# Optimization experiments

Hardware: AMD Instinct MI355X
Metric: run time of the kernel (lower is better)

## Reference

```python
import jax, jax.numpy as jnp
import numpy as np

D_IN = 4097   # 4096 obj feat + 1 depth
D_H1 = 512
D_H2 = 256
N_HEADS = 4
D_HEAD = D_H2 // N_HEADS
D_FF = 512


def setup_inputs() -> dict:
    key = jax.random.key(0)
    ks = jax.random.split(key, 20)
    B, T, N = 2, 100, 30
    s = lambda *sh: 1.0 / np.sqrt(sh[0])
    inp = {
        "object_features": jax.random.normal(ks[0], (B, T, N, 4096), jnp.float32),
        "object_depths": jax.random.uniform(ks[1], (B, T, N, 1), jnp.float32),
        # spatial encoder (2-layer fully-connected message passing)
        "W1a": jax.random.normal(ks[2], (D_IN, D_H1), jnp.float32) * s(D_IN),
        "W2a": jax.random.normal(ks[3], (D_IN, D_H1), jnp.float32) * s(D_IN),
        "b1a": jnp.zeros((D_H1,), jnp.float32),
        "W1b": jax.random.normal(ks[4], (D_H1, D_H2), jnp.float32) * s(D_H1),
        "W2b": jax.random.normal(ks[5], (D_H1, D_H2), jnp.float32) * s(D_H1),
        "b1b": jnp.zeros((D_H2,), jnp.float32),
        # temporal transformer encoder layer (post-LN)
        "Wq": jax.random.normal(ks[6], (D_H2, D_H2), jnp.float32) * s(D_H2),
        "Wk": jax.random.normal(ks[7], (D_H2, D_H2), jnp.float32) * s(D_H2),
        "Wv": jax.random.normal(ks[8], (D_H2, D_H2), jnp.float32) * s(D_H2),
        "Wo": jax.random.normal(ks[9], (D_H2, D_H2), jnp.float32) * s(D_H2),
        "ln1_g": jnp.ones((D_H2,), jnp.float32),
        "ln1_b": jnp.zeros((D_H2,), jnp.float32),
        "Wf1": jax.random.normal(ks[10], (D_H2, D_FF), jnp.float32) * s(D_H2),
        "bf1": jnp.zeros((D_FF,), jnp.float32),
        "Wf2": jax.random.normal(ks[11], (D_FF, D_H2), jnp.float32) * s(D_FF),
        "bf2": jnp.zeros((D_H2,), jnp.float32),
        "ln2_g": jnp.ones((D_H2,), jnp.float32),
        "ln2_b": jnp.zeros((D_H2,), jnp.float32),
        # classifier
        "Wc": jax.random.normal(ks[12], (D_H2, 1), jnp.float32) * s(D_H2),
        "bc": jnp.zeros((1,), jnp.float32),
    }
    return inp


def _layer_norm(x, g, b, eps=1e-5):
    mu = jnp.mean(x, axis=-1, keepdims=True)
    var = jnp.var(x, axis=-1, keepdims=True)
    return (x - mu) * jax.lax.rsqrt(var + eps) * g + b


def _forward(object_features, object_depths, W1a, W2a, b1a, W1b, W2b, b1b,
             Wq, Wk, Wv, Wo, ln1_g, ln1_b, Wf1, bf1, Wf2, bf2, ln2_g, ln2_b,
             Wc, bc):
    B, T, N, _ = object_features.shape
    x = jnp.concatenate([object_features, object_depths], axis=-1)  # (B,T,N,4097)
    # fully-connected graph (torch.combinations, both directions):
    # aggregated message for node i = mean over all j != i.
    def mp(h, Ws, Wn, b):
        neigh = (jnp.sum(h, axis=2, keepdims=True) - h) / (N - 1)
        return jax.nn.relu(h @ Ws + neigh @ Wn + b)
    h = mp(x, W1a, W2a, b1a)      # (B,T,N,512)
    h = mp(h, W1b, W2b, b1b)      # (B,T,N,256)
    g = jnp.mean(h, axis=2)       # global mean pool -> (B,T,256)
    # temporal transformer encoder (self-attention over T, post-LN)
    q = (g @ Wq).reshape(B, T, N_HEADS, D_HEAD)
    k = (g @ Wk).reshape(B, T, N_HEADS, D_HEAD)
    v = (g @ Wv).reshape(B, T, N_HEADS, D_HEAD)
    scores = jnp.einsum("bthd,bshd->bhts", q, k) / np.sqrt(D_HEAD)
    attn = jax.nn.softmax(scores, axis=-1)
    ctx = jnp.einsum("bhts,bshd->bthd", attn, v).reshape(B, T, D_H2) @ Wo
    y = _layer_norm(g + ctx, ln1_g, ln1_b)
    ff = jax.nn.relu(y @ Wf1 + bf1) @ Wf2 + bf2
    z = _layer_norm(y + ff, ln2_g, ln2_b)  # (B,T,256)
    # dropout is identity in eval mode -> probs2 == probs, uncertainty == 0
    logits = (z @ Wc + bc).squeeze(-1)     # (B,T)
    probs = jax.nn.sigmoid(logits)
    uncertainty = jnp.zeros_like(probs)
    return probs, uncertainty


def reference(object_features, object_depths, W1a, W2a, b1a, W1b, W2b, b1b,
              Wq, Wk, Wv, Wo, ln1_g, ln1_b, Wf1, bf1, Wf2, bf2, ln2_g, ln2_b,
              Wc, bc):
    return _forward(object_features, object_depths, W1a, W2a, b1a, W1b, W2b,
                    b1b, Wq, Wk, Wv, Wo, ln1_g, ln1_b, Wf1, bf1, Wf2, bf2,
                    ln2_g, ln2_b, Wc, bc)
```

## Files before the change

### kernel.cpp

```cpp
#include <hip/hip_runtime.h>
#include <hip/hip_bf16.h>
#include <stdint.h>

typedef unsigned short u16;
typedef __attribute__((ext_vector_type(8))) short short8;
typedef __attribute__((ext_vector_type(4))) float floatx4;
typedef __attribute__((ext_vector_type(4))) unsigned short ushort4_t;

#define BT 200
#define NOBJ 30
#define KP2 4224
#define DIN 4097
#define DH1 512
#define DH2 256
#define DFF 512
#define MPAD 6016
#define CHZ 176
#define NBIGW (132*16)
#define NSMALL 512
#define NCONV (BT*3)
#define NZERO 128

__device__ __forceinline__ u16 f2bf(float f) {
    union { float f; uint32_t u; } c; c.f = f;
    uint32_t u = c.u;
    u += 0x7FFF + ((u >> 16) & 1);
    return (u16)(u >> 16);
}

__device__ __forceinline__ void load16_lds(const u16* g, u16* l) {
    __builtin_amdgcn_global_load_lds(
        (const __attribute__((address_space(1))) void*)g,
        (__attribute__((address_space(3))) void*)l, 16, 0, 0);
}

__device__ __forceinline__ size_t tile_off(int ytile, int row, int c8) {
    int z = c8 / CHZ, rem = c8 - z * CHZ;
    int i = rem >> 3, kw = rem & 7;
    int ks = kw ^ (row & 7);
    return ((((size_t)(ytile * 3 + z) * 22 + i) * 128 + row) * 64) + ks * 8;
}

__global__ void prep_all(const float* __restrict__ W1a, const float* __restrict__ W2a,
                         const float* __restrict__ W1b, const float* __restrict__ W2b,
                         const float* __restrict__ feat, const float* __restrict__ depth,
                         u16* __restrict__ Wc1T, u16* __restrict__ W2aTs,
                         u16* __restrict__ Wc2T, u16* __restrict__ W2bTs,
                         u16* __restrict__ XbT, u16* __restrict__ SbT,
                         float* __restrict__ zeroBase, size_t zeroQuads) {
    __shared__ float t1[32][33];
    __shared__ float t2[32][33];
    int bid = blockIdx.x, tid = threadIdx.x;
    if (bid < NCONV) {
        int bt = bid / 3;
        int c8 = (bid % 3) * 256 + tid;
        if (c8 >= 528) return;
        int k8 = c8 * 8;
        int zc = c8 / CHZ, rem = c8 - zc * CHZ;
        int ic = rem >> 3, kwc = rem & 7;
        float s[8] = {};
        if (k8 < 4096) {
            const float* fb = feat + (size_t)bt * NOBJ * 4096 + k8;
            #pragma unroll 1
            for (int n0 = 0; n0 < NOBJ; n0 += 6) {
                float4 va[6], vb[6];
                #pragma unroll
                for (int u = 0; u < 6; u++) {
                    const float* p = fb + (size_t)(n0 + u) * 4096;
                    va[u] = *(const float4*)p;
                    vb[u] = *(const float4*)(p + 4);
                }
                #pragma unroll
                for (int u = 0; u < 6; u++) {
                    int r = bt * NOBJ + n0 + u;
                    float v[8] = {va[u].x, va[u].y, va[u].z, va[u].w,
                                  vb[u].x, vb[u].y, vb[u].z, vb[u].w};
                    short8 o;
                    #pragma unroll
                    for (int e = 0; e < 8; e++) { s[e] += v[e]; o[e] = (short)f2bf(v[e]); }
                    size_t off = ((((size_t)((r >> 7) * 3 + zc) * 22 + ic) * 128
                                   + (r & 127)) * 64) + (size_t)(kwc ^ (r & 7)) * 8;
                    *(short8*)(XbT + off) = o;
                }
            }
        } else {
            for (int n = 0; n < NOBJ; n++) {
                int r = bt * NOBJ + n;
                short8 o = {};
                if (k8 == 4096) {
                    float d = depth[r];
                    s[0] += d;
                    o[0] = (short)f2bf(d);
                }
                size_t off = ((((size_t)((r >> 7) * 3 + zc) * 22 + ic) * 128
                               + (r & 127)) * 64) + (size_t)(kwc ^ (r & 7)) * 8;
                *(short8*)(XbT + off) = o;
            }
        }
        short8 so;
        #pragma unroll
        for (int e = 0; e < 8; e++) so[e] = (short)f2bf(s[e]);
        {
            int r = bt;
            size_t off = ((((size_t)((r >> 7) * 3 + zc) * 22 + ic) * 128
                           + (r & 127)) * 64) + (size_t)(kwc ^ (r & 7)) * 8;
            *(short8*)(SbT + off) = so;
        }
    } else if (bid < NCONV + NZERO) {
        int zid = bid - NCONV;
        float4* p = (float4*)zeroBase;
        float4 zz = {0.f, 0.f, 0.f, 0.f};
        for (size_t idx = (size_t)zid * 256 + tid; idx < zeroQuads; idx += (size_t)NZERO * 256)
            p[idx] = zz;
    } else if (bid < NCONV + NZERO + NSMALL) {
        int idx = (bid - NCONV - NZERO) * 256 + tid;
        int j = idx >> 9, k = idx & 511;
        float a = W1b[k * DH2 + j];
        float b = W2b[k * DH2 + j] * (1.f / 29.f);
        Wc2T[j * DH1 + k]  = f2bf(a - b);
        W2bTs[j * DH1 + k] = f2bf(b);
    } else {
        int b2 = bid - NCONV - NZERO - NSMALL;
        int kb = (b2 % 132) * 32, jb = (b2 / 132) * 32;
        int tx = tid & 31, ty = tid >> 5;
        #pragma unroll
        for (int r = 0; r < 32; r += 8) {
            int k = kb + ty + r, j = jb + tx;
            float a = 0.f, b = 0.f;
            if (k < DIN) { a = W1a[k * DH1 + j]; b = W2a[k * DH1 + j]; }
            float bs = b * (1.f / 29.f);
            t1[ty + r][tx] = a - bs;
            t2[ty + r][tx] = bs;
        }
        __syncthreads();
        #pragma unroll
        for (int r = 0; r < 32; r += 8) {
            int j = jb + ty + r, k = kb + tx;
            int x = j >> 7, row = j & 127;
            size_t off = tile_off(x, row, k >> 3) + (k & 7);
            Wc1T[off]  = f2bf(t1[tx][ty + r]);
            W2aTs[off] = f2bf(t2[tx][ty + r]);
        }
    }
}

__global__ __launch_bounds__(256) void gemmA(
    const u16* __restrict__ XbT, const u16* __restrict__ WaT,
    const u16* __restrict__ SbT, const u16* __restrict__ WsT,
    float* __restrict__ hacc, float* __restrict__ uOut) {
    __shared__ __align__(16) u16 Al[8192];
    __shared__ __align__(16) u16 Bl[8192];
    int bid = blockIdx.x;
    const u16 *Abase, *Bbase;
    float* outF;
    int m0, n0, M;
    if (bid < 564) {
        int xcd = bid & 7, slot = bid >> 3;
        int lid = (xcd < 4 ? xcd * 71 : 284 + (xcd - 4) * 70) + slot;
        int x = lid & 3, y = (lid >> 2) % 47, z = lid / 188;
        Abase = XbT + (size_t)((y * 3 + z) * 22) * 8192;
        Bbase = WaT + (size_t)((x * 3 + z) * 22) * 8192;
        outF = hacc; M = 6000; m0 = y * 128; n0 = x * 128;
    } else {
        int rem = bid - 564;
        int x = rem & 3, y = (rem >> 2) & 1, z = rem >> 3;
        Abase = SbT + (size_t)((y * 3 + z) * 22) * 8192;
        Bbase = WsT + (size_t)((x * 3 + z) * 22) * 8192;
        outF = uOut; M = BT; m0 = y * 128; n0 = x * 128;
    }
    int tid = threadIdx.x, lane = tid & 63, w = tid >> 6;
    floatx4 acc[4][4] = {};
    int lrow = lane & 15, q = lane >> 4;
    int wm = (w & 1) * 64, wn = (w >> 1) * 64;
    int swz = lrow & 7;

    for (int i = 0; i < 22; i++) {
        const u16* as = Abase + (size_t)i * 8192;
        const u16* bs = Bbase + (size_t)i * 8192;
        #pragma unroll
        for (int it = 0; it < 4; it++) {
            load16_lds(as + (it * 256 + tid) * 8, Al + it * 2048 + w * 512);
            load16_lds(bs + (it * 256 + tid) * 8, Bl + it * 2048 + w * 512);
        }
        __syncthreads();
        #pragma unroll
        for (int h = 0; h < 2; h++) {
            int ci = h * 4 + q;
            int so = (ci ^ swz) * 8;
            short8 af[4], bfv[4];
            #pragma unroll
            for (int ii = 0; ii < 4; ii++)
                af[ii] = *(short8*)(Al + (wm + ii * 16 + lrow) * 64 + so);
            #pragma unroll
            for (int j = 0; j < 4; j++)
                bfv[j] = *(short8*)(Bl + (wn + j * 16 + lrow) * 64 + so);
            #pragma unroll
            for (int ii = 0; ii < 4; ii++)
                #pragma unroll
                for (int j = 0; j < 4; j++)
                    acc[ii][j] = __builtin_amdgcn_mfma_f32_16x16x32_bf16(af[ii], bfv[j], acc[ii][j], 0, 0, 0);
        }
        __syncthreads();
    }

    #pragma unroll
    for (int ii = 0; ii < 4; ii++)
        #pragma unroll
        for (int j = 0; j < 4; j++)
            #pragma unroll
            for (int r = 0; r < 4; r++) {
                int row = m0 + wm + ii * 16 + q * 4 + r;
                int col = n0 + wn + j * 16 + lrow;
                if (row < M)
                    atomicAdd(&outF[(size_t)row * DH1 + col], acc[ii][j][r]);
            }
}

__global__ __launch_bounds__(256) void gemmB(
    const u16* __restrict__ hb, const u16* __restrict__ Wc2T,
    const u16* __restrict__ Shb, const u16* __restrict__ W2bTs,
    float* __restrict__ hacc2, float* __restrict__ u2Out) {
    __shared__ __align__(16) u16 Al[64 * 64];
    __shared__ __align__(16) u16 Bl[128 * 64];
    int bid = blockIdx.x;
    const u16 *A, *B;
    float* outF;
    int m0, n0, kbeg, M;
    if (bid < 376) {
        int xcd = bid & 7, slot = bid >> 3;
        int lid = xcd * 47 + slot;
        int x = lid & 1, y = (lid >> 1) % 94, z = lid / 188;
        A = hb; B = Wc2T; outF = hacc2; M = 6000;
        m0 = y * 64; n0 = x * 128; kbeg = z * 256;
    } else {
        int rem = bid - 376;
        int x = rem & 1, y = (rem >> 1) & 3, z = rem >> 3;
        A = Shb; B = W2bTs; outF = u2Out; M = BT;
        m0 = y * 64; n0 = x * 128; kbeg = z * 256;
    }
    int kend = kbeg + 256;
    const int N = DH2, K = DH1;
    int tid = threadIdx.x;
    int lane = tid & 63, w = tid >> 6;
    int srow = tid >> 3, kslot = tid & 7;
    floatx4 acc[2][4] = {};
    int lrow = lane & 15, q = lane >> 4;
    int wm = (w & 1) * 32, wn = (w >> 1) * 64;
    int swz = lrow & 7;

    for (int kb = kbeg; kb < kend; kb += 64) {
        #pragma unroll
        for (int it = 0; it < 2; it++) {
            int row = it * 32 + srow;
            int kph = kslot ^ (row & 7);
            load16_lds(A + (size_t)(m0 + row) * K + kb + kph * 8,
                       Al + it * 2048 + w * 512);
        }
        #pragma unroll
        for (int it = 0; it < 4; it++) {
            int row = it * 32 + srow;
            int kph = kslot ^ (row & 7);
            load16_lds(B + (size_t)(n0 + row) * K + kb + kph * 8,
                       Bl + it * 2048 + w * 512);
        }
        __syncthreads();
        #pragma unroll
        for (int h = 0; h < 2; h++) {
            int ci = h * 4 + q;
            int so = (ci ^ swz) * 8;
            short8 af[2], bfv[4];
            #pragma unroll
            for (int i = 0; i < 2; i++)
                af[i] = *(short8*)(Al + (wm + i * 16 + lrow) * 64 + so);
            #pragma unroll
            for (int j = 0; j < 4; j++)
                bfv[j] = *(short8*)(Bl + (wn + j * 16 + lrow) * 64 + so);
            #pragma unroll
            for (int i = 0; i < 2; i++)
                #pragma unroll
                for (int j = 0; j < 4; j++)
                    acc[i][j] = __builtin_amdgcn_mfma_f32_16x16x32_bf16(af[i], bfv[j], acc[i][j], 0, 0, 0);
        }
        __syncthreads();
    }

    #pragma unroll
    for (int i = 0; i < 2; i++)
        #pragma unroll
        for (int j = 0; j < 4; j++)
            #pragma unroll
            for (int r = 0; r < 4; r++) {
                int row = m0 + wm + i * 16 + q * 4 + r;
                int col = n0 + wn + j * 16 + lrow;
                if (row < M)
                    atomicAdd(&outF[(size_t)row * N + col], acc[i][j][r]);
            }
}

__global__ void reduce1(const float* __restrict__ hacc, const float* __restrict__ u,
                        const float* __restrict__ b1a,
                        u16* __restrict__ hb, u16* __restrict__ Shb) {
    __shared__ float sl[128];
    int bt = blockIdx.x, c0 = blockIdx.y * 128;
    int lc = threadIdx.x & 127, rp = threadIdx.x >> 7;
    int col = c0 + lc;
    float ub = u[bt * DH1 + col] + b1a[col];
    float s = 0.f;
    for (int n = rp; n < NOBJ; n += 2) {
        float v = hacc[(size_t)(bt * NOBJ + n) * DH1 + col] + ub;
        v = v > 0.f ? v : 0.f;
        hb[(size_t)(bt * NOBJ + n) * DH1 + col] = f2bf(v);
        s += v;
    }
    if (rp == 0) sl[lc] = s;
    __syncthreads();
    if (rp == 1) Shb[bt * DH1 + col] = f2bf(sl[lc] + s);
}

__global__ void reduce2_qkv(const float* __restrict__ hacc2, const float* __restrict__ u2,
                            const float* __restrict__ b1b,
                            const float* __restrict__ Wq, const float* __restrict__ Wk,
                            const float* __restrict__ Wv,
                            float* __restrict__ g, float* __restrict__ q,
                            float* __restrict__ k, float* __restrict__ v) {
    __shared__ float gl[DH2];
    int bt = blockIdx.x, j = threadIdx.x;
    float ub = u2[bt * DH2 + j] + b1b[j];
    float a = 0.f;
    for (int n = 0; n < NOBJ; n++) {
        float vv = hacc2[(size_t)(bt * NOBJ + n) * DH2 + j] + ub;
        a += vv > 0.f ? vv : 0.f;
    }
    a *= (1.f / 30.f);
    gl[j] = a;
    g[bt * DH2 + j] = a;
    __syncthreads();
    float aq = 0.f, ak = 0.f, av = 0.f;
    for (int kk = 0; kk < DH2; kk++) {
        float x = gl[kk];
        aq += x * Wq[kk * DH2 + j];
        ak += x * Wk[kk * DH2 + j];
        av += x * Wv[kk * DH2 + j];
    }
    q[bt * DH2 + j] = aq;
    k[bt * DH2 + j] = ak;
    v[bt * DH2 + j] = av;
}

__device__ __forceinline__ float block_sum256(float v, volatile float* red) {
    #pragma unroll
    for (int o = 32; o > 0; o >>= 1) v += __shfl_down(v, o);
    int w = threadIdx.x >> 6;
    __syncthreads();
    if ((threadIdx.x & 63) == 0) red[w] = v;
    __syncthreads();
    return red[0] + red[1] + red[2] + red[3];
}

__global__ void attn_head(const float* __restrict__ qg, const float* __restrict__ kg,
                          const float* __restrict__ vg, const float* __restrict__ g,
                          const float* __restrict__ Wo,
                          const float* __restrict__ ln1g, const float* __restrict__ ln1b,
                          const float* __restrict__ Wf1, const float* __restrict__ bf1,
                          const float* __restrict__ Wf2, const float* __restrict__ bf2,
                          const float* __restrict__ ln2g, const float* __restrict__ ln2b,
                          const float* __restrict__ Wc, const float* __restrict__ bc,
                          float* __restrict__ out) {
    __shared__ float ql[DH2];
    __shared__ float scl[4][128];
    __shared__ float ctxl[DH2];
    __shared__ float yl[DH2];
    __shared__ float ffl[DFF];
    __shared__ float red[4];
    int row = blockIdx.x, tid = threadIdx.x;
    int base = (row >= 100) ? 100 : 0;
    ql[tid] = qg[row * DH2 + tid];
    __syncthreads();

    for (int p = tid; p < 512; p += 256) {
        int h = p >> 7, s = p & 127;
        if (s < 100) {
            const float* kr = kg + (size_t)(base + s) * DH2 + h * 64;
            float a = 0.f;
            #pragma unroll 8
            for (int d = 0; d < 64; d++) a += ql[h * 64 + d] * kr[d];
            scl[h][s] = a * 0.125f;
        }
    }
    __syncthreads();

    {
        int w = tid >> 6, lane = tid & 63;
        int s2 = 64 + lane;
        float a  = scl[w][lane];
        float b2 = (s2 < 100) ? scl[w][s2] : -1e30f;
        float m = fmaxf(a, b2);
        #pragma unroll
        for (int o = 32; o > 0; o >>= 1) m = fmaxf(m, __shfl_down(m, o));
        m = __shfl(m, 0);
        float e1 = __expf(a - m);
        float e2 = (s2 < 100) ? __expf(b2 - m) : 0.f;
        float sm = e1 + e2;
        #pragma unroll
        for (int o = 32; o > 0; o >>= 1) sm += __shfl_down(sm, o);
        sm = __shfl(sm, 0);
        float r = 1.f / sm;
        scl[w][lane] = e1 * r;
        if (s2 < 100) scl[w][s2] = e2 * r;
    }
    __syncthreads();

    {
        int h = tid >> 6;
        float o = 0.f;
        for (int s = 0; s < 100; s++)
            o += scl[h][s] * vg[(size_t)(base + s) * DH2 + tid];
        ctxl[tid] = o;
    }
    __syncthreads();

    float o = 0.f;
    for (int kk = 0; kk < DH2; kk++) o += ctxl[kk] * Wo[kk * DH2 + tid];
    float t = g[row * DH2 + tid] + o;
    float mu  = block_sum256(t, red) * (1.f / DH2);
    float ex2 = block_sum256(t * t, red) * (1.f / DH2);
    float y = (t - mu) * rsqrtf(ex2 - mu * mu + 1e-5f) * ln1g[tid] + ln1b[tid];
    yl[tid] = y;
    __syncthreads();
    for (int jj = tid; jj < DFF; jj += 256) {
        float a = bf1[jj];
        for (int kk = 0; kk < DH2; kk++) a += yl[kk] * Wf1[kk * DFF + jj];
        ffl[jj] = a > 0.f ? a : 0.f;
    }
    __syncthreads();
    float o2 = bf2[tid];
    for (int kk = 0; kk < DFF; kk++) o2 += ffl[kk] * Wf2[kk * DH2 + tid];
    float z0 = y + o2;
    float mu2  = block_sum256(z0, red) * (1.f / DH2);
    float ex22 = block_sum256(z0 * z0, red) * (1.f / DH2);
    float z = (z0 - mu2) * rsqrtf(ex22 - mu2 * mu2 + 1e-5f) * ln2g[tid] + ln2b[tid];
    float logit = block_sum256(z * Wc[tid], red) + bc[0];
    if (tid == 0) {
        out[row]      = 1.f / (1.f + __expf(-logit));
        out[BT + row] = 0.f;
    }
}

extern "C" void kernel_launch(void* const* d_in, const int* in_sizes, int n_in,
                              void* d_out, int out_size, void* d_ws, size_t ws_size,
                              hipStream_t stream) {
    const float* feat  = (const float*)d_in[0];
    const float* depth = (const float*)d_in[1];
    const float* W1a = (const float*)d_in[2];
    const float* W2a = (const float*)d_in[3];
    const float* b1a = (const float*)d_in[4];
    const float* W1b = (const float*)d_in[5];
    const float* W2b = (const float*)d_in[6];
    const float* b1b = (const float*)d_in[7];
    const float* Wq  = (const float*)d_in[8];
    const float* Wk  = (const float*)d_in[9];
    const float* Wv  = (const float*)d_in[10];
    const float* Wo  = (const float*)d_in[11];
    const float* ln1g = (const float*)d_in[12];
    const float* ln1b = (const float*)d_in[13];
    const float* Wf1 = (const float*)d_in[14];
    const float* bf1 = (const float*)d_in[15];
    const float* Wf2 = (const float*)d_in[16];
    const float* bf2 = (const float*)d_in[17];
    const float* ln2g = (const float*)d_in[18];
    const float* ln2b = (const float*)d_in[19];
    const float* Wc  = (const float*)d_in[20];
    const float* bc  = (const float*)d_in[21];
    float* out = (float*)d_out;
    char* ws = (char*)d_ws;

    size_t off = 0;
    u16* XbT   = (u16*)(ws + off); off += (size_t)MPAD * KP2 * 2;
    u16* SbT   = (u16*)(ws + off); off += (size_t)256 * KP2 * 2;
    u16* Wc1T  = (u16*)(ws + off); off += (size_t)DH1 * KP2 * 2;
    u16* W2aTs = (u16*)(ws + off); off += (size_t)DH1 * KP2 * 2;
    u16* Wc2T  = (u16*)(ws + off); off += (size_t)DH2 * DH1 * 2;
    u16* W2bTs = (u16*)(ws + off); off += (size_t)DH2 * DH1 * 2;
    u16* Shb   = (u16*)(ws + off); off += (size_t)256 * DH1 * 2;
    char* zBase = ws + off;
    float* hacc  = (float*)(ws + off); off += (size_t)6000 * DH1 * 4;
    float* hacc2 = (float*)(ws + off); off += (size_t)6000 * DH2 * 4;
    float* u     = (float*)(ws + off); off += (size_t)BT * DH1 * 4;
    float* u2    = (float*)(ws + off); off += (size_t)BT * DH2 * 4;
    size_t zeroQuads = (size_t)(ws + off - zBase) / 16;
    u16* hb = XbT;
    float* g = (float*)SbT;
    float* q = g + BT * DH2;
    float* k = q + BT * DH2;
    float* v = k + BT * DH2;

    prep_all<<<NBIGW + NSMALL + NCONV + NZERO, 256, 0, stream>>>(
        W1a, W2a, W1b, W2b, feat, depth,
        Wc1T, W2aTs, Wc2T, W2bTs, XbT, SbT, (float*)zBase, zeroQuads);
    gemmA<<<564 + 24, 256, 0, stream>>>(XbT, Wc1T, SbT, W2aTs, hacc, u);
    reduce1<<<dim3(BT, 4), 256, 0, stream>>>(hacc, u, b1a, hb, Shb);
    gemmB<<<376 + 16, 256, 0, stream>>>(hb, Wc2T, Shb, W2bTs, hacc2, u2);
    reduce2_qkv<<<BT, DH2, 0, stream>>>(hacc2, u2, b1b, Wq, Wk, Wv, g, q, k, v);
    attn_head<<<BT, DH2, 0, stream>>>(q, k, v, g, Wo, ln1g, ln1b, Wf1, bf1,
                                      Wf2, bf2, ln2g, ln2b, Wc, bc, out);
}
```

Before: 376.3 us.

## Replace split-K atomic accumulation with per-slice partial buffers summed in reducers

The split-K GEMMs now write plain stores into separate partial-sum buffers, one per K slice, instead of doing atomicAdd into a shared zero-initialised accumulator. The reduce kernels then sum the three (or two) partial slices. This removes the large zero-fill in the prep kernel and the atomic traffic. In exchange the workspace grows and the reducers read more data. hacc2P aliases haccP, which is safe because reduce1 has already consumed haccP before gemmB writes to it.

```diff
diff --git a/kernel.cpp b/kernel.cpp
--- a/kernel.cpp
+++ b/kernel.cpp
@@ -19,7 +19,10 @@
 #define NBIGW (132*16)
 #define NSMALL 512
 #define NCONV (BT*3)
-#define NZERO 128
+#define NZERO 16
+
+#define PSTR1 ((size_t)6000 * DH1)
+#define PSTR2 ((size_t)6000 * DH2)
 
 __device__ __forceinline__ u16 f2bf(float f) {
     union { float f; uint32_t u; } c; c.f = f;
@@ -147,26 +150,28 @@
 __global__ __launch_bounds__(256) void gemmA(
     const u16* __restrict__ XbT, const u16* __restrict__ WaT,
     const u16* __restrict__ SbT, const u16* __restrict__ WsT,
-    float* __restrict__ hacc, float* __restrict__ uOut) {
+    float* __restrict__ haccP, float* __restrict__ uOut) {
     __shared__ __align__(16) u16 Al[8192];
     __shared__ __align__(16) u16 Bl[8192];
     int bid = blockIdx.x;
     const u16 *Abase, *Bbase;
     float* outF;
     int m0, n0, M;
+    bool useAtomic;
     if (bid < 564) {
         int xcd = bid & 7, slot = bid >> 3;
         int lid = (xcd < 4 ? xcd * 71 : 284 + (xcd - 4) * 70) + slot;
         int x = lid & 3, y = (lid >> 2) % 47, z = lid / 188;
         Abase = XbT + (size_t)((y * 3 + z) * 22) * 8192;
         Bbase = WaT + (size_t)((x * 3 + z) * 22) * 8192;
-        outF = hacc; M = 6000; m0 = y * 128; n0 = x * 128;
+        outF = haccP + (size_t)z * PSTR1;
+        M = 6000; m0 = y * 128; n0 = x * 128; useAtomic = false;
     } else {
         int rem = bid - 564;
         int x = rem & 3, y = (rem >> 2) & 1, z = rem >> 3;
         Abase = SbT + (size_t)((y * 3 + z) * 22) * 8192;
         Bbase = WsT + (size_t)((x * 3 + z) * 22) * 8192;
-        outF = uOut; M = BT; m0 = y * 128; n0 = x * 128;
+        outF = uOut; M = BT; m0 = y * 128; n0 = x * 128; useAtomic = true;
     }
     int tid = threadIdx.x, lane = tid & 63, w = tid >> 6;
     floatx4 acc[4][4] = {};
@@ -203,40 +208,56 @@
         __syncthreads();
     }
 
-    #pragma unroll
-    for (int ii = 0; ii < 4; ii++)
-        #pragma unroll
-        for (int j = 0; j < 4; j++)
-            #pragma unroll
-            for (int r = 0; r < 4; r++) {
-                int row = m0 + wm + ii * 16 + q * 4 + r;
-                int col = n0 + wn + j * 16 + lrow;
-                if (row < M)
-                    atomicAdd(&outF[(size_t)row * DH1 + col], acc[ii][j][r]);
-            }
+    if (useAtomic) {
+        #pragma unroll
+        for (int ii = 0; ii < 4; ii++)
+            #pragma unroll
+            for (int j = 0; j < 4; j++)
+                #pragma unroll
+                for (int r = 0; r < 4; r++) {
+                    int row = m0 + wm + ii * 16 + q * 4 + r;
+                    int col = n0 + wn + j * 16 + lrow;
+                    if (row < M)
+                        atomicAdd(&outF[(size_t)row * DH1 + col], acc[ii][j][r]);
+                }
+    } else {
+        #pragma unroll
+        for (int ii = 0; ii < 4; ii++)
+            #pragma unroll
+            for (int j = 0; j < 4; j++)
+                #pragma unroll
+                for (int r = 0; r < 4; r++) {
+                    int row = m0 + wm + ii * 16 + q * 4 + r;
+                    int col = n0 + wn + j * 16 + lrow;
+                    if (row < M)
+                        outF[(size_t)row * DH1 + col] = acc[ii][j][r];
+                }
+    }
 }
 
 __global__ __launch_bounds__(256) void gemmB(
     const u16* __restrict__ hb, const u16* __restrict__ Wc2T,
     const u16* __restrict__ Shb, const u16* __restrict__ W2bTs,
-    float* __restrict__ hacc2, float* __restrict__ u2Out) {
+    float* __restrict__ hacc2P, float* __restrict__ u2Out) {
     __shared__ __align__(16) u16 Al[64 * 64];
     __shared__ __align__(16) u16 Bl[128 * 64];
     int bid = blockIdx.x;
     const u16 *A, *B;
     float* outF;
     int m0, n0, kbeg, M;
+    bool useAtomic;
     if (bid < 376) {
         int xcd = bid & 7, slot = bid >> 3;
         int lid = xcd * 47 + slot;
         int x = lid & 1, y = (lid >> 1) % 94, z = lid / 188;
-        A = hb; B = Wc2T; outF = hacc2; M = 6000;
-        m0 = y * 64; n0 = x * 128; kbeg = z * 256;
+        A = hb; B = Wc2T; M = 6000;
+        outF = hacc2P + (size_t)z * PSTR2;
+        m0 = y * 64; n0 = x * 128; kbeg = z * 256; useAtomic = false;
     } else {
         int rem = bid - 376;
         int x = rem & 1, y = (rem >> 1) & 3, z = rem >> 3;
         A = Shb; B = W2bTs; outF = u2Out; M = BT;
-        m0 = y * 64; n0 = x * 128; kbeg = z * 256;
+        m0 = y * 64; n0 = x * 128; kbeg = z * 256; useAtomic = true;
     }
     int kend = kbeg + 256;
     const int N = DH2, K = DH1;
@@ -284,20 +305,34 @@
         __syncthreads();
     }
 
-    #pragma unroll
-    for (int i = 0; i < 2; i++)
-        #pragma unroll
-        for (int j = 0; j < 4; j++)
-            #pragma unroll
-            for (int r = 0; r < 4; r++) {
-                int row = m0 + wm + i * 16 + q * 4 + r;
-                int col = n0 + wn + j * 16 + lrow;
-                if (row < M)
-                    atomicAdd(&outF[(size_t)row * N + col], acc[i][j][r]);
-            }
-}
-
-__global__ void reduce1(const float* __restrict__ hacc, const float* __restrict__ u,
+    if (useAtomic) {
+        #pragma unroll
+        for (int i = 0; i < 2; i++)
+            #pragma unroll
+            for (int j = 0; j < 4; j++)
+                #pragma unroll
+                for (int r = 0; r < 4; r++) {
+                    int row = m0 + wm + i * 16 + q * 4 + r;
+                    int col = n0 + wn + j * 16 + lrow;
+                    if (row < M)
+                        atomicAdd(&outF[(size_t)row * N + col], acc[i][j][r]);
+                }
+    } else {
+        #pragma unroll
+        for (int i = 0; i < 2; i++)
+            #pragma unroll
+            for (int j = 0; j < 4; j++)
+                #pragma unroll
+                for (int r = 0; r < 4; r++) {
+                    int row = m0 + wm + i * 16 + q * 4 + r;
+                    int col = n0 + wn + j * 16 + lrow;
+                    if (row < M)
+                        outF[(size_t)row * N + col] = acc[i][j][r];
+                }
+    }
+}
+
+__global__ void reduce1(const float* __restrict__ haccP, const float* __restrict__ u,
                         const float* __restrict__ b1a,
                         u16* __restrict__ hb, u16* __restrict__ Shb) {
     __shared__ float sl[128];
@@ -307,9 +342,10 @@
     float ub = u[bt * DH1 + col] + b1a[col];
     float s = 0.f;
     for (int n = rp; n < NOBJ; n += 2) {
-        float v = hacc[(size_t)(bt * NOBJ + n) * DH1 + col] + ub;
+        size_t idx = (size_t)(bt * NOBJ + n) * DH1 + col;
+        float v = haccP[idx] + haccP[idx + PSTR1] + haccP[idx + 2 * PSTR1] + ub;
         v = v > 0.f ? v : 0.f;
-        hb[(size_t)(bt * NOBJ + n) * DH1 + col] = f2bf(v);
+        hb[idx] = f2bf(v);
         s += v;
     }
     if (rp == 0) sl[lc] = s;
@@ -317,7 +353,7 @@
     if (rp == 1) Shb[bt * DH1 + col] = f2bf(sl[lc] + s);
 }
 
-__global__ void reduce2_qkv(const float* __restrict__ hacc2, const float* __restrict__ u2,
+__global__ void reduce2_qkv(const float* __restrict__ hacc2P, const float* __restrict__ u2,
                             const float* __restrict__ b1b,
                             const float* __restrict__ Wq, const float* __restrict__ Wk,
                             const float* __restrict__ Wv,
@@ -328,7 +364,8 @@
     float ub = u2[bt * DH2 + j] + b1b[j];
     float a = 0.f;
     for (int n = 0; n < NOBJ; n++) {
-        float vv = hacc2[(size_t)(bt * NOBJ + n) * DH2 + j] + ub;
+        size_t idx = (size_t)(bt * NOBJ + n) * DH2 + j;
+        float vv = hacc2P[idx] + hacc2P[idx + PSTR2] + ub;
         a += vv > 0.f ? vv : 0.f;
     }
     a *= (1.f / 30.f);
@@ -483,11 +520,11 @@
     u16* W2bTs = (u16*)(ws + off); off += (size_t)DH2 * DH1 * 2;
     u16* Shb   = (u16*)(ws + off); off += (size_t)256 * DH1 * 2;
     char* zBase = ws + off;
-    float* hacc  = (float*)(ws + off); off += (size_t)6000 * DH1 * 4;
-    float* hacc2 = (float*)(ws + off); off += (size_t)6000 * DH2 * 4;
     float* u     = (float*)(ws + off); off += (size_t)BT * DH1 * 4;
     float* u2    = (float*)(ws + off); off += (size_t)BT * DH2 * 4;
     size_t zeroQuads = (size_t)(ws + off - zBase) / 16;
+    float* haccP  = (float*)(ws + off); off += 3 * PSTR1 * 4;
+    float* hacc2P = haccP;
     u16* hb = XbT;
     float* g = (float*)SbT;
     float* q = g + BT * DH2;
@@ -497,10 +534,10 @@
     prep_all<<<NBIGW + NSMALL + NCONV + NZERO, 256, 0, stream>>>(
         W1a, W2a, W1b, W2b, feat, depth,
         Wc1T, W2aTs, Wc2T, W2bTs, XbT, SbT, (float*)zBase, zeroQuads);
-    gemmA<<<564 + 24, 256, 0, stream>>>(XbT, Wc1T, SbT, W2aTs, hacc, u);
-    reduce1<<<dim3(BT, 4), 256, 0, stream>>>(hacc, u, b1a, hb, Shb);
-    gemmB<<<376 + 16, 256, 0, stream>>>(hb, Wc2T, Shb, W2bTs, hacc2, u2);
-    reduce2_qkv<<<BT, DH2, 0, stream>>>(hacc2, u2, b1b, Wq, Wk, Wv, g, q, k, v);
+    gemmA<<<564 + 24, 256, 0, stream>>>(XbT, Wc1T, SbT, W2aTs, haccP, u);
+    reduce1<<<dim3(BT, 4), 256, 0, stream>>>(haccP, u, b1a, hb, Shb);
+    gemmB<<<376 + 16, 256, 0, stream>>>(hb, Wc2T, Shb, W2bTs, hacc2P, u2);
+    reduce2_qkv<<<BT, DH2, 0, stream>>>(hacc2P, u2, b1b, Wq, Wk, Wv, g, q, k, v);
     attn_head<<<BT, DH2, 0, stream>>>(q, k, v, g, Wo, ln1g, ln1b, Wf1, bf1,
                                       Wf2, bf2, ln2g, ln2b, Wc, bc, out);
 }
```

New measurement: 354.8 us. -5.7%, faster.
